# Kernel optimization log

Measured on AMD Instinct MI355X. Metric: run time of the kernel, lower is better.

Reference implementation:

```python
import jax, jax.numpy as jnp
import numpy as np

NUM_LEVELS = 8
CODEBOOK_SIZE = 1024
D_MODEL = 512


def setup_inputs() -> dict:
    key = jax.random.key(0)
    kx, kc = jax.random.split(key)
    x = jax.random.normal(kx, (8, 4096, D_MODEL), dtype=jnp.float32)
    # stacked embedding tables, one per RVQ level: [L, K, D]
    codebooks = jax.random.normal(kc, (NUM_LEVELS, CODEBOOK_SIZE, D_MODEL), dtype=jnp.float32)
    return {"x": x, "codebooks": codebooks}


def reference(x, codebooks):
    """Residual VQ: per level, nearest-codebook lookup on the residual.

    x: [B, N, D], codebooks: [L, K, D].
    Returns (quantized [B, N, D] with straight-through estimator, indices [B, N, L]).
    """
    residual = x
    q_sum = jnp.zeros_like(x)
    all_indices = []
    for l in range(codebooks.shape[0]):
        cb = codebooks[l]  # [K, D]
        # squared Euclidean distance; argmin matches torch.cdist argmin
        r2 = jnp.sum(residual * residual, axis=-1, keepdims=True)      # [B, N, 1]
        c2 = jnp.sum(cb * cb, axis=-1)                                  # [K]
        cross = jnp.einsum("bnd,kd->bnk", residual, cb)                # [B, N, K]
        dist2 = r2 - 2.0 * cross + c2                                   # [B, N, K]
        idx = jnp.argmin(dist2, axis=-1)                                # [B, N]
        all_indices.append(idx)
        q = cb[idx]                                                     # gather: [B, N, D]
        q_sum = q_sum + q
        residual = residual - q
    # straight-through: forward value is q_sum, gradient flows to x only
    quantized = x + jax.lax.stop_gradient(q_sum - x)
    return quantized, jnp.stack(all_indices, axis=-1)
```

## Files before the change

### kernel.cpp

```cpp
#include <hip/hip_runtime.h>
#include <stdint.h>

#define NLV 8
#define KCB 1024
#define DM  512
#define NTOK (8*4096)
#define BETA 0.00390625f

typedef _Float16 f16;
typedef f16  f16x4 __attribute__((ext_vector_type(4)));
typedef f16  f16x8 __attribute__((ext_vector_type(8)));
typedef float f32x4 __attribute__((ext_vector_type(4)));

typedef __attribute__((address_space(1))) const unsigned int* as1p;
typedef __attribute__((address_space(3))) unsigned int*       as3p;
__device__ __forceinline__ void gll16(const void* g, void* l) {
    __builtin_amdgcn_global_load_lds((as1p)g, (as3p)l, 16, 0, 0);
}

__global__ void c2_kernel(const float* __restrict__ cbs, float* __restrict__ c2) {
    int row  = blockIdx.x;
    int lane = threadIdx.x;
    const float4* p4 = (const float4*)(cbs + (size_t)row * DM);
    float4 a = p4[lane];
    float4 b = p4[lane + 64];
    float s = a.x*a.x + a.y*a.y + a.z*a.z + a.w*a.w
            + b.x*b.x + b.y*b.y + b.z*b.z + b.w*b.w;
    float t = (float)(f16)a.x + (float)(f16)a.y + (float)(f16)a.z + (float)(f16)a.w
            + (float)(f16)b.x + (float)(f16)b.y + (float)(f16)b.z + (float)(f16)b.w;
    #pragma unroll
    for (int off = 32; off > 0; off >>= 1) {
        s += __shfl_down(s, off, 64);
        t += __shfl_down(t, off, 64);
    }
    if (lane == 0) c2[row] = s + 2.0f * BETA * t;
}

__global__ void split_kernel(const float* __restrict__ src,
                             f16* __restrict__ hi, f16* __restrict__ lo) {
    size_t i = (size_t)blockIdx.x * 256 + threadIdx.x;
    float4 v = ((const float4*)src)[i];
    f16x4 h, l;
    h.x = (f16)v.x; l.x = (f16)((v.x - (float)h.x) + BETA);
    h.y = (f16)v.y; l.y = (f16)((v.y - (float)h.y) + BETA);
    h.z = (f16)v.z; l.z = (f16)((v.z - (float)h.z) + BETA);
    h.w = (f16)v.w; l.w = (f16)((v.w - (float)h.w) + BETA);
    ((f16x4*)hi)[i] = h;
    ((f16x4*)lo)[i] = l;
}

#define MBT  128
#define NCH  256
#define KS   32
#define NTHR 512
#define BUFB 49152

__global__ __launch_bounds__(NTHR, 2)
void rvq_mfma(const float* __restrict__ xin, float* __restrict__ qout,
              const float* __restrict__ cbs,
              const f16* __restrict__ Bhi, const f16* __restrict__ Blo,
              f16* __restrict__ Ahi, f16* __restrict__ Alo,
              const float* __restrict__ c2g, float* __restrict__ idxout,
              int lvl, int is_last)
{
    __shared__ char smem[3 * BUFB];
    const int tid  = threadIdx.x;
    const int lane = tid & 63;
    const int w    = tid >> 6;
    const int wn   = w & 3;
    const int wm   = w >> 2;
    const int tx   = lane & 15;
    const int q    = lane >> 4;
    const size_t tok0 = (size_t)blockIdx.x * MBT;

    const f16*   Bh_l = Bhi + (size_t)lvl * KCB * DM;
    const f16*   Bl_l = Blo + (size_t)lvl * KCB * DM;
    const float* c2l  = c2g + lvl * KCB;
    const float* cbl  = cbs + (size_t)lvl * KCB * DM;

    const int rloc = lane >> 2;
    const int sg   = (lane & 3) ^ ((lane >> 3) & 3);
    const int rsw  = q ^ ((tx >> 1) & 3);

    const f16* pAh = Ahi + (tok0 + w * 16 + rloc) * (size_t)DM + sg * 8;
    const f16* pAl = Alo + (tok0 + w * 16 + rloc) * (size_t)DM + sg * 8;
    const size_t bRow = (size_t)(w * 16 + rloc) * DM + sg * 8;

    auto stage = [&](char* buf, int gk2) {
        const int ko    = (gk2 & 15) * KS;
        const size_t bo = (size_t)((gk2 >> 4) * NCH) * DM + ko;
        gll16(pAh + ko, buf + w * 1024);
        gll16(pAl + ko, buf + 8192 + w * 1024);
        gll16(Bh_l + bo + bRow,            buf + 16384 + w * 1024);
        gll16(Bh_l + bo + bRow + 128 * DM, buf + 16384 + (w + 8) * 1024);
        gll16(Bl_l + bo + bRow,            buf + 32768 + w * 1024);
        gll16(Bl_l + bo + bRow + 128 * DM, buf + 32768 + (w + 8) * 1024);
    };

    int aoff[4], boff[4];
    #pragma unroll
    for (int i = 0; i < 4; ++i) aoff[i] = (wm * 64 + i * 16 + tx) * 64 + rsw * 16;
    #pragma unroll
    for (int j = 0; j < 4; ++j) boff[j] = (wn * 64 + j * 16 + tx) * 64 + rsw * 16;

    float bestv[16];
    int   besti[16];
    #pragma unroll
    for (int t = 0; t < 16; ++t) { bestv[t] = 3.4e38f; besti[t] = 0; }

    f16x8 ahE[4], bhE[4], ahO[4], bhO[4];

    stage(smem, 0);
    __syncthreads();
    stage(smem + BUFB, 1);
    #pragma unroll
    for (int i = 0; i < 4; ++i) ahE[i] = *(const f16x8*)(smem + aoff[i]);
    #pragma unroll
    for (int j = 0; j < 4; ++j) bhE[j] = *(const f16x8*)(smem + 16384 + boff[j]);

    auto kbody = [&](int gk, f32x4 (&acc)[4][4],
                     f16x8 (&ahC)[4], f16x8 (&bhC)[4],
                     f16x8 (&ahN)[4], f16x8 (&bhN)[4]) {
        char* bufC = smem + (gk % 3) * BUFB;
        char* bufR = smem + ((gk + 1) % 3) * BUFB;
        char* bufS = smem + ((gk + 2) % 3) * BUFB;

        __syncthreads();
        if (gk + 2 < 64) stage(bufS, gk + 2);

        f16x8 al[4], bl[4];
        #pragma unroll
        for (int i = 0; i < 4; ++i) al[i] = *(const f16x8*)(bufC + 8192 + aoff[i]);
        #pragma unroll
        for (int j = 0; j < 4; ++j) bl[j] = *(const f16x8*)(bufC + 32768 + boff[j]);

        if (gk + 1 < 64) {
            #pragma unroll
            for (int i = 0; i < 4; ++i) ahN[i] = *(const f16x8*)(bufR + aoff[i]);
            #pragma unroll
            for (int j = 0; j < 4; ++j) bhN[j] = *(const f16x8*)(bufR + 16384 + boff[j]);
        }
        __builtin_amdgcn_sched_barrier(0);

        __builtin_amdgcn_s_setprio(1);
        #pragma unroll
        for (int j = 0; j < 4; ++j)
            #pragma unroll
            for (int i = 0; i < 4; ++i)
                acc[i][j] = __builtin_amdgcn_mfma_f32_16x16x32_f16(ahC[i], bhC[j], acc[i][j], 0, 0, 0);
        #pragma unroll
        for (int j = 0; j < 4; ++j)
            #pragma unroll
            for (int i = 0; i < 4; ++i)
                acc[i][j] = __builtin_amdgcn_mfma_f32_16x16x32_f16(ahC[i], bl[j], acc[i][j], 0, 0, 0);
        #pragma unroll
        for (int j = 0; j < 4; ++j)
            #pragma unroll
            for (int i = 0; i < 4; ++i)
                acc[i][j] = __builtin_amdgcn_mfma_f32_16x16x32_f16(al[i], bhC[j], acc[i][j], 0, 0, 0);
        __builtin_amdgcn_s_setprio(0);
    };

    for (int ch = 0; ch < KCB / NCH; ++ch) {
        f32x4 acc[4][4];
        #pragma unroll
        for (int i = 0; i < 4; ++i)
            #pragma unroll
            for (int j = 0; j < 4; ++j) acc[i][j] = (f32x4)0.0f;

        for (int kp = 0; kp < 8; ++kp) {
            const int gk = ch * 16 + kp * 2;
            kbody(gk,     acc, ahE, bhE, ahO, bhO);
            kbody(gk + 1, acc, ahO, bhO, ahE, bhE);
        }

        const int cb0 = ch * NCH;
        #pragma unroll
        for (int j = 0; j < 4; ++j) {
            int n = cb0 + wn * 64 + j * 16 + tx;
            float c2v = c2l[n];
            #pragma unroll
            for (int i = 0; i < 4; ++i)
                #pragma unroll
                for (int r = 0; r < 4; ++r) {
                    float s = fmaf(-2.f, acc[i][j][r], c2v);
                    int t = i * 4 + r;
                    if (s < bestv[t]) { bestv[t] = s; besti[t] = n; }
                }
        }
    }

    #pragma unroll
    for (int t = 0; t < 16; ++t) {
        float v = bestv[t]; int bi = besti[t];
        #pragma unroll
        for (int off = 1; off < 16; off <<= 1) {
            float ov = __shfl_xor(v, off, 64);
            int   oi = __shfl_xor(bi, off, 64);
            if (ov < v || (ov == v && oi < bi)) { v = ov; bi = oi; }
        }
        bestv[t] = v; besti[t] = bi;
    }

    float* redV = (float*)smem;
    int*   redI = (int*)(smem + 2048);
    int*   kbst = (int*)(smem + 4096);
    __syncthreads();
    if (tx == 0) {
        #pragma unroll
        for (int i = 0; i < 4; ++i)
            #pragma unroll
            for (int r = 0; r < 4; ++r) {
                int m = wm * 64 + i * 16 + q * 4 + r;
                redV[wn * 128 + m] = bestv[i * 4 + r];
                redI[wn * 128 + m] = besti[i * 4 + r];
            }
    }
    __syncthreads();
    if (tid < MBT) {
        float bv = redV[tid]; int bi = redI[tid];
        #pragma unroll
        for (int ww = 1; ww < 4; ++ww) {
            float v  = redV[ww * 128 + tid];
            int   ii = redI[ww * 128 + tid];
            if (v < bv || (v == bv && ii < bi)) { bv = v; bi = ii; }
        }
        kbst[tid] = bi;
        idxout[(tok0 + tid) * NLV + lvl] = (float)bi;
    }
    __syncthreads();

    #pragma unroll 4
    for (int it = 0; it < 16; ++it) {
        int e  = it * NTHR + tid;
        int t  = e >> 6, d8 = e & 63;
        size_t go = (tok0 + t) * (size_t)DM + d8 * 8;
        f16x8 h8 = *(const f16x8*)&Ahi[go];
        f16x8 l8 = *(const f16x8*)&Alo[go];
        const float* cp = &cbl[(size_t)kbst[t] * DM + d8 * 8];
        float4 c0 = *(const float4*)cp;
        float4 c1 = *(const float4*)(cp + 4);
        float r[8];
        r[0] = (float)h8[0] + ((float)l8[0] - BETA) - c0.x;
        r[1] = (float)h8[1] + ((float)l8[1] - BETA) - c0.y;
        r[2] = (float)h8[2] + ((float)l8[2] - BETA) - c0.z;
        r[3] = (float)h8[3] + ((float)l8[3] - BETA) - c0.w;
        r[4] = (float)h8[4] + ((float)l8[4] - BETA) - c1.x;
        r[5] = (float)h8[5] + ((float)l8[5] - BETA) - c1.y;
        r[6] = (float)h8[6] + ((float)l8[6] - BETA) - c1.z;
        r[7] = (float)h8[7] + ((float)l8[7] - BETA) - c1.w;
        if (is_last) {
            float4 x0 = *(const float4*)&xin[go];
            float4 x1 = *(const float4*)&xin[go + 4];
            float4 q0 = make_float4(x0.x - r[0], x0.y - r[1], x0.z - r[2], x0.w - r[3]);
            float4 q1 = make_float4(x1.x - r[4], x1.y - r[5], x1.z - r[6], x1.w - r[7]);
            *(float4*)&qout[go]     = q0;
            *(float4*)&qout[go + 4] = q1;
        } else {
            f16x8 h, l;
            #pragma unroll
            for (int k = 0; k < 8; ++k) {
                h[k] = (f16)r[k];
                l[k] = (f16)((r[k] - (float)h[k]) + BETA);
            }
            *(f16x8*)&Ahi[go] = h;
            *(f16x8*)&Alo[go] = l;
        }
    }
}

extern "C" void kernel_launch(void* const* d_in, const int* in_sizes, int n_in,
                              void* d_out, int out_size, void* d_ws, size_t ws_size,
                              hipStream_t stream) {
    const float* x   = (const float*)d_in[0];
    const float* cbs = (const float*)d_in[1];
    float* qout   = (float*)d_out;
    float* idxout = qout + (size_t)NTOK * DM;

    const size_t B_ELE = (size_t)NLV * KCB * DM;
    const size_t A_ELE = (size_t)NTOK * DM;

    f16* Bhi = (f16*)d_ws;
    f16* Blo = Bhi + B_ELE;
    f16* Ahi = Blo + B_ELE;
    f16* Alo = Ahi + A_ELE;
    float* c2 = (float*)(Alo + A_ELE);

    split_kernel<<<(int)(B_ELE / 4 / 256), 256, 0, stream>>>(cbs, Bhi, Blo);
    split_kernel<<<(int)(A_ELE / 4 / 256), 256, 0, stream>>>(x, Ahi, Alo);
    c2_kernel<<<NLV * KCB, 64, 0, stream>>>(cbs, c2);

    const int nblocks = NTOK / MBT;
    for (int l = 0; l < NLV; ++l) {
        rvq_mfma<<<nblocks, NTHR, 0, stream>>>(x, qout, cbs,
                                               Bhi, Blo, Ahi, Alo, c2, idxout,
                                               l, (l == NLV - 1) ? 1 : 0);
    }
}
```

Baseline: 1.117 ms.

## Interleave staged global loads and LDS reads between MFMA phases with fine-grained barriers

Splits each k-step into three MFMA phases and interleaves the global-to-LDS staging of A, B-hi and B-lo tiles and the LDS fragment reads between them. Each phase is separated by raw s_barriers and sched_barriers, with a manual vmcnt wait replacing the single __syncthreads. The prologue now issues two stages before the first sync. The aim is to spread memory traffic across the compute so the MFMA pipes stay busier. In exchange it adds many more barriers per step and relies on hand-set vmcnt counts, which risks stalls or subtle races on the triple buffer.

```diff
diff --git a/kernel.cpp b/kernel.cpp
--- a/kernel.cpp
+++ b/kernel.cpp
@@ -17,6 +17,10 @@
 __device__ __forceinline__ void gll16(const void* g, void* l) {
     __builtin_amdgcn_global_load_lds((as1p)g, (as3p)l, 16, 0, 0);
 }
+
+#define VMCNT(n) asm volatile("s_waitcnt vmcnt(" #n ")" ::: "memory")
+#define SBAR()   __builtin_amdgcn_s_barrier()
+#define SCHED0() __builtin_amdgcn_sched_barrier(0)
 
 __global__ void c2_kernel(const float* __restrict__ cbs, float* __restrict__ c2) {
     int row  = blockIdx.x;
@@ -86,7 +90,7 @@
     const f16* pAl = Alo + (tok0 + w * 16 + rloc) * (size_t)DM + sg * 8;
     const size_t bRow = (size_t)(w * 16 + rloc) * DM + sg * 8;
 
-    auto stage = [&](char* buf, int gk2) {
+    auto stageAll = [&](char* buf, int gk2) {
         const int ko    = (gk2 & 15) * KS;
         const size_t bo = (size_t)((gk2 >> 4) * NCH) * DM + ko;
         gll16(pAh + ko, buf + w * 1024);
@@ -110,9 +114,9 @@
 
     f16x8 ahE[4], bhE[4], ahO[4], bhO[4];
 
-    stage(smem, 0);
+    stageAll(smem, 0);
+    stageAll(smem + BUFB, 1);
     __syncthreads();
-    stage(smem + BUFB, 1);
     #pragma unroll
     for (int i = 0; i < 4; ++i) ahE[i] = *(const f16x8*)(smem + aoff[i]);
     #pragma unroll
@@ -122,43 +126,65 @@
                      f16x8 (&ahC)[4], f16x8 (&bhC)[4],
                      f16x8 (&ahN)[4], f16x8 (&bhN)[4]) {
         char* bufC = smem + (gk % 3) * BUFB;
-        char* bufR = smem + ((gk + 1) % 3) * BUFB;
+        char* bufN = smem + ((gk + 1) % 3) * BUFB;
         char* bufS = smem + ((gk + 2) % 3) * BUFB;
-
-        __syncthreads();
-        if (gk + 2 < 64) stage(bufS, gk + 2);
-
-        f16x8 al[4], bl[4];
-        #pragma unroll
-        for (int i = 0; i < 4; ++i) al[i] = *(const f16x8*)(bufC + 8192 + aoff[i]);
+        const bool doStage = (gk + 2 < 64);
+        const int ko    = ((gk + 2) & 15) * KS;
+        const size_t bo = (size_t)(((gk + 2) >> 4) * NCH) * DM + ko;
+
+        if (doStage) {
+            gll16(pAh + ko, bufS + w * 1024);
+            gll16(pAl + ko, bufS + 8192 + w * 1024);
+        }
+        f16x8 bl[4], al[4];
         #pragma unroll
         for (int j = 0; j < 4; ++j) bl[j] = *(const f16x8*)(bufC + 32768 + boff[j]);
-
-        if (gk + 1 < 64) {
-            #pragma unroll
-            for (int i = 0; i < 4; ++i) ahN[i] = *(const f16x8*)(bufR + aoff[i]);
-            #pragma unroll
-            for (int j = 0; j < 4; ++j) bhN[j] = *(const f16x8*)(bufR + 16384 + boff[j]);
-        }
-        __builtin_amdgcn_sched_barrier(0);
-
+        SBAR(); SCHED0();
         __builtin_amdgcn_s_setprio(1);
         #pragma unroll
         for (int j = 0; j < 4; ++j)
             #pragma unroll
             for (int i = 0; i < 4; ++i)
                 acc[i][j] = __builtin_amdgcn_mfma_f32_16x16x32_f16(ahC[i], bhC[j], acc[i][j], 0, 0, 0);
+        __builtin_amdgcn_s_setprio(0);
+        SBAR(); SCHED0();
+
+        if (doStage) {
+            gll16(Bh_l + bo + bRow,            bufS + 16384 + w * 1024);
+            gll16(Bh_l + bo + bRow + 128 * DM, bufS + 16384 + (w + 8) * 1024);
+        }
+        #pragma unroll
+        for (int i = 0; i < 4; ++i) al[i] = *(const f16x8*)(bufC + 8192 + aoff[i]);
+        SBAR(); SCHED0();
+        __builtin_amdgcn_s_setprio(1);
         #pragma unroll
         for (int j = 0; j < 4; ++j)
             #pragma unroll
             for (int i = 0; i < 4; ++i)
                 acc[i][j] = __builtin_amdgcn_mfma_f32_16x16x32_f16(ahC[i], bl[j], acc[i][j], 0, 0, 0);
+        __builtin_amdgcn_s_setprio(0);
+        VMCNT(4);
+        SBAR(); SCHED0();
+
+        if (doStage) {
+            gll16(Bl_l + bo + bRow,            bufS + 32768 + w * 1024);
+            gll16(Bl_l + bo + bRow + 128 * DM, bufS + 32768 + (w + 8) * 1024);
+        }
+        if (gk + 1 < 64) {
+            #pragma unroll
+            for (int i = 0; i < 4; ++i) ahN[i] = *(const f16x8*)(bufN + aoff[i]);
+            #pragma unroll
+            for (int j = 0; j < 4; ++j) bhN[j] = *(const f16x8*)(bufN + 16384 + boff[j]);
+        }
+        SBAR(); SCHED0();
+        __builtin_amdgcn_s_setprio(1);
         #pragma unroll
         for (int j = 0; j < 4; ++j)
             #pragma unroll
             for (int i = 0; i < 4; ++i)
                 acc[i][j] = __builtin_amdgcn_mfma_f32_16x16x32_f16(al[i], bhC[j], acc[i][j], 0, 0, 0);
         __builtin_amdgcn_s_setprio(0);
+        SBAR(); SCHED0();
     };
 
     for (int ch = 0; ch < KCB / NCH; ++ch) {
```

Result: slower. 1.236 ms (+10.6%).
